# Kernel optimization log

Measured on AMD Instinct MI355X. Metric: run time of the kernel, lower is better.

Reference implementation:

```python
import jax, jax.numpy as jnp
import numpy as np

B, S, T = 64, 64, 20
E, H, V, K = 512, 1024, 32000, 100
L, W = 50, 8
NEG = -1e9


def lstm_cell(x, h, c, Wih, Whh, bih, bhh):
    # PyTorch gate order: input, forget, cell, output
    g = x @ Wih.T + h @ Whh.T + bih + bhh
    i, f, gg, o = jnp.split(g, 4, axis=-1)
    c = jax.nn.sigmoid(f) * c + jax.nn.sigmoid(i) * jnp.tanh(gg)
    h = jax.nn.sigmoid(o) * jnp.tanh(c)
    return h, c


def setup_inputs():
    key = jax.random.key(0)
    ks = jax.random.split(key, 32)
    rn = lambda k, shp, s=0.02: (s * jax.random.normal(k, shp)).astype(jnp.float32)
    embed_W = jax.random.normal(ks[0], (V, E), dtype=jnp.float32).at[0].set(0.0)  # padding_idx 0
    return {
        'src_seqs': jax.random.randint(ks[1], (B, S), 1, V),
        'src_lengths': jax.random.randint(ks[2], (B,), S // 2, S + 1),
        'trg_seqs': jax.random.randint(ks[3], (B, T), 1, V),
        'ctc_seqs': jax.random.randint(ks[4], (B, L, W), 1, V),
        'ctc_lengths': jax.random.randint(ks[5], (B,), 1, L + 1),
        'embed_W': embed_W,
        'enc_Wih': rn(ks[6], (4 * H, E)), 'enc_Whh': rn(ks[7], (4 * H, H)),
        'enc_bih': rn(ks[8], (4 * H,)), 'enc_bhh': rn(ks[9], (4 * H,)),
        'dec_Wih': rn(ks[10], (4 * H, E + H)), 'dec_Whh': rn(ks[11], (4 * H, H)),
        'dec_bih': rn(ks[12], (4 * H,)), 'dec_bhh': rn(ks[13], (4 * H,)),
        'qk_W': rn(ks[14], (K, E)), 'qk_b': rn(ks[15], (K,)),
        'qv_W': rn(ks[16], (H, E)), 'qv_b': rn(ks[17], (H,)),
        'ak_W': rn(ks[18], (K, H)), 'ak_b': rn(ks[19], (K,)),
        'out_W': rn(ks[20], (E, 2 * H)), 'out_b': rn(ks[21], (E,)),
        'wd_b': rn(ks[22], (V,)),
        'hf1_W': rn(ks[23], (2 * H, H)), 'hf1_b': rn(ks[24], (2 * H,)),
        'hf2_W': rn(ks[25], (H, 2 * H)), 'hf2_b': rn(ks[26], (H,)),
        'cf1_W': rn(ks[27], (2 * H, H)), 'cf1_b': rn(ks[28], (2 * H,)),
        'cf2_W': rn(ks[29], (H, 2 * H)), 'cf2_b': rn(ks[30], (H,)),
    }


def forward(floats, ints):
    (embed_W, enc_Wih, enc_Whh, enc_bih, enc_bhh, dec_Wih, dec_Whh, dec_bih, dec_bhh,
     qk_W, qk_b, qv_W, qv_b, ak_W, ak_b, out_W, out_b, wd_b,
     hf1_W, hf1_b, hf2_W, hf2_b, cf1_W, cf1_b, cf2_W, cf2_b) = floats
    src_seqs, src_lengths, trg_seqs, ctc_seqs, ctc_lengths = ints

    src_embed = embed_W[src_seqs]  # [B,S,E]

    # ---- encoder LSTM (seq-first scan); packed-seq final state = state at src_lengths-1 ----
    def enc_step(carry, x_t):
        h, c = lstm_cell(x_t, carry[0], carry[1], enc_Wih, enc_Whh, enc_bih, enc_bhh)
        return (h, c), (h, c)
    z = jnp.zeros((B, H), jnp.float32)
    _, (hs, cs) = jax.lax.scan(enc_step, (z, z), src_embed.transpose(1, 0, 2))  # [S,B,H]
    idx = src_lengths - 1
    h_last = hs[idx, jnp.arange(B)]
    c_last = cs[idx, jnp.arange(B)]

    # ---- init_hidden: MLP transforms of encoder final state ----
    h0 = jax.nn.relu(h_last @ hf1_W.T + hf1_b) @ hf2_W.T + hf2_b
    c0 = jax.nn.relu(c_last @ cf1_W.T + cf1_b) @ cf2_W.T + cf2_b

    # ---- persona context: mean word embedding per context item ----
    ctx_embed = embed_W[ctc_seqs].mean(axis=2)       # [B,L,E]
    q_key = jnp.tanh(ctx_embed @ qk_W.T + qk_b)      # [B,L,K]
    q_value = ctx_embed @ qv_W.T + qv_b              # [B,L,H]
    mask = jnp.arange(L)[None, :] < ctc_lengths[:, None]  # [B,L]

    ans_embed = embed_W[trg_seqs]                    # [B,T,E]

    # ---- decoder: per-step attention + LSTM + tied-vocab projection ----
    def dec_step(carry, x_t):
        h, c = carry
        a_key = jnp.tanh(h @ ak_W.T + ak_b)                      # [B,K]
        e = jnp.einsum('blk,bk->bl', q_key, a_key)
        w = jax.nn.softmax(jnp.where(mask, e, NEG), axis=1)
        ctx = jnp.einsum('bl,blh->bh', w, q_value)               # [B,H]
        h, c = lstm_cell(jnp.concatenate([x_t, ctx], -1), h, c,
                         dec_Wih, dec_Whh, dec_bih, dec_bhh)
        ox = jnp.concatenate([h, ctx], -1) @ out_W.T + out_b     # [B,E]
        logits = ox @ embed_W.T + wd_b                           # tied weights, [B,V]
        return (h, c), logits

    # teacher forcing (sampling_rate=1.0, T-1 <= max_len-2)
    _, logits = jax.lax.scan(dec_step, (h0, c0), ans_embed[:, :T - 1].transpose(1, 0, 2))
    return logits.transpose(1, 0, 2)  # [B, T-1, V]


def reference(src_seqs, src_lengths, trg_seqs, ctc_seqs, ctc_lengths, embed_W, enc_Wih, enc_Whh, enc_bih, enc_bhh, dec_Wih, dec_Whh, dec_bih, dec_bhh, qk_W, qk_b, qv_W, qv_b, ak_W, ak_b, out_W, out_b, wd_b, hf1_W, hf1_b, hf2_W, hf2_b, cf1_W, cf1_b, cf2_W, cf2_b):
    floats = (embed_W, enc_Wih, enc_Whh, enc_bih, enc_bhh, dec_Wih, dec_Whh, dec_bih, dec_bhh,
              qk_W, qk_b, qv_W, qv_b, ak_W, ak_b, out_W, out_b, wd_b,
              hf1_W, hf1_b, hf2_W, hf2_b, cf1_W, cf1_b, cf2_W, cf2_b)
    ints = (src_seqs, src_lengths, trg_seqs, ctc_seqs, ctc_lengths)
    return forward(floats, ints)
```

## Files before the change

### kernel.cpp

```cpp
#include <hip/hip_runtime.h>
#include <hip/hip_bf16.h>
#include <math.h>

#define Bn 64
#define Sn 64
#define Tn 20
#define TD 19
#define En 512
#define Hn 1024
#define Vn 32000
#define Kan 100
#define Lnn 50
#define Wnn 8

typedef __attribute__((ext_vector_type(8))) short short8v;
typedef __attribute__((ext_vector_type(4))) float floatx4;
typedef __hip_bfloat16 bf16;
typedef unsigned long long ull;

__device__ __forceinline__ float sigm(float x) { return 1.0f / (1.0f + expf(-x)); }
__device__ __forceinline__ float bfb2f(unsigned int u) {
    return __builtin_bit_cast(float, u << 16);
}
__device__ __forceinline__ unsigned short f2bfb(float f) {
    return __builtin_bit_cast(unsigned short, __float2bfloat16(f));
}

#define ALOAD(p)     __hip_atomic_load((p), __ATOMIC_RELAXED, __HIP_MEMORY_SCOPE_AGENT)
#define ASTORE(p, v) __hip_atomic_store((p), (v), __ATOMIC_RELAXED, __HIP_MEMORY_SCOPE_AGENT)

__device__ __forceinline__ uint4 gload16(const void* p) {
    uint4 v;
    asm volatile("global_load_dwordx4 %0, %1, off sc0 sc1"
                 : "=v"(v) : "v"(p));
    return v;
}
#define GWAIT() asm volatile("s_waitcnt vmcnt(0)" ::: "memory")

__device__ __forceinline__ void gbar(unsigned int* c, int tid) {
    __builtin_amdgcn_sched_barrier(0);
    __syncthreads();
    if (tid == 0) {
        __hip_atomic_fetch_add(c, 1u, __ATOMIC_RELAXED, __HIP_MEMORY_SCOPE_AGENT);
        while (__hip_atomic_load(c, __ATOMIC_RELAXED, __HIP_MEMORY_SCOPE_AGENT) < 128u) {
            __builtin_amdgcn_s_sleep(1);
        }
    }
    __syncthreads();
    __builtin_amdgcn_sched_barrier(0);
}

#define EOFF(r, p) (((r) << 5) + ((((p) ^ ((r) & 3))) << 3))

__device__ __forceinline__ int aswz(int row, int p) {
    return row * 32 + (((p ^ ((row >> 1) & 3))) << 3);
}
__device__ __forceinline__ int wswz(int col, int s, int K) {
    return col * K + (((s & ~7) | ((s & 7) ^ (col & 7))) << 3);
}

template<int GATHER, int EPI, int ACT>
__global__ __launch_bounds__(256)
void mgemm(const bf16* __restrict__ A, int lda, const int* __restrict__ tok,
           const bf16* __restrict__ W, int ldw,
           const float* __restrict__ b1, const float* __restrict__ b2,
           float* __restrict__ C, int ldc,
           bf16* __restrict__ Cbf, int ldcbf,
           int M, int N, int K)
{
    __shared__ bf16 As[128 * 32];
    __shared__ bf16 Bs[128 * 32];
    const int tid = threadIdx.x;
    const int lane = tid & 63, wv = tid >> 6;
    const int wm = wv >> 1, wn = wv & 1;
    const int n0 = (EPI == 2 ? blockIdx.y : blockIdx.x) * 128;
    const int r0 = (EPI == 2 ? blockIdx.x : blockIdx.y) * 128;
    const int srow = tid >> 2, sp = tid & 3;

    const int ra_r0 = r0 + srow, ra_r1 = r0 + srow + 64;
    const bool av0 = ra_r0 < M, av1 = ra_r1 < M;
    const size_t arow0 = (size_t)(av0 ? (GATHER ? tok[ra_r0] : ra_r0) : 0) * lda;
    const size_t arow1 = (size_t)(av1 ? (GATHER ? tok[ra_r1] : ra_r1) : 0) * lda;
    const size_t wrow0 = (size_t)(n0 + srow) * ldw;
    const size_t wrow1 = (size_t)(n0 + srow + 64) * ldw;

    const uint4 z4 = make_uint4(0, 0, 0, 0);
    uint4 ra0, ra1, rb0, rb1;
#define LOADTILE_G(k0) do { \
        ra0 = av0 ? *((const uint4*)(A + arow0 + (k0)) + sp) : z4; \
        ra1 = av1 ? *((const uint4*)(A + arow1 + (k0)) + sp) : z4; \
        rb0 = *((const uint4*)(W + wrow0 + (k0)) + sp); \
        rb1 = *((const uint4*)(W + wrow1 + (k0)) + sp); \
    } while (0)

    floatx4 acc[4][4] = {};
    const int lr = lane & 15, p2 = lane >> 4;

    LOADTILE_G(0);
    for (int k0 = 0; k0 < K; k0 += 32) {
        __syncthreads();
        *(uint4*)(As + EOFF(srow, sp)) = ra0;
        *(uint4*)(As + EOFF(srow + 64, sp)) = ra1;
        *(uint4*)(Bs + EOFF(srow, sp)) = rb0;
        *(uint4*)(Bs + EOFF(srow + 64, sp)) = rb1;
        __syncthreads();
        if (k0 + 32 < K) LOADTILE_G(k0 + 32);
        short8v aF[4], bF[4];
#pragma unroll
        for (int mf = 0; mf < 4; ++mf)
            aF[mf] = *(const short8v*)(As + EOFF(wm * 64 + mf * 16 + lr, p2));
#pragma unroll
        for (int nf = 0; nf < 4; ++nf)
            bF[nf] = *(const short8v*)(Bs + EOFF(wn * 64 + nf * 16 + lr, p2));
#pragma unroll
        for (int mf = 0; mf < 4; ++mf)
#pragma unroll
            for (int nf = 0; nf < 4; ++nf)
                acc[mf][nf] = __builtin_amdgcn_mfma_f32_16x16x32_bf16(
                    aF[mf], bF[nf], acc[mf][nf], 0, 0, 0);
    }
#undef LOADTILE_G

    const int rbase = r0 + wm * 64 + (lane >> 4) * 4;
    const int nbase = n0 + wn * 64 + (lane & 15);
#pragma unroll
    for (int nf = 0; nf < 4; ++nf) {
        const int n = nbase + nf * 16;
        if (n >= N) continue;
        float bias = b1 ? b1[n] : 0.0f;
        if (b2) bias += b2[n];
#pragma unroll
        for (int mf = 0; mf < 4; ++mf) {
#pragma unroll
            for (int i = 0; i < 4; ++i) {
                const int r = rbase + mf * 16 + i;
                if (r >= M) continue;
                float v = acc[mf][nf][i] + bias;
                if (ACT == 1) v = tanhf(v);
                if (ACT == 2) v = fmaxf(v, 0.0f);
                if (EPI == 2) {
                    int b = r & 63, t = r >> 6;
                    C[(size_t)(b * TD + t) * Vn + n] = v;
                } else {
                    if (C) C[(size_t)r * ldc + n] = v;
                    if (Cbf) Cbf[(size_t)r * ldcbf + n] = __float2bfloat16(v);
                }
            }
        }
    }
}

struct EncP {
    const bf16* Wp;
    const bf16* Xg;
    bf16* hA; bf16* hB;
    const int* len;
    bf16* hlast; bf16* clast;
    unsigned int* cnt;
};

__global__ __launch_bounds__(512, 1)
void enc_persist(EncP p)
{
    __shared__ bf16 Ws_l[32 * 1024];
    __shared__ bf16 Asb[2][64 * 32];
    __shared__ float Gs[64][33];
    const int tid = threadIdx.x;
    const int lane = tid & 63, wv = tid >> 6;
    const int mf = wv >> 1, nf = wv & 1;
    const int blk = blockIdx.x;
    const int n0 = blk * 32;

    for (int idx = tid; idx < 32 * 128; idx += 512) {
        int col = idx >> 7, s = idx & 127;
        uint4 v = *(const uint4*)(p.Wp + (size_t)(n0 + col) * 1024 + s * 8);
        *(uint4*)(Ws_l + wswz(col, s, 1024)) = v;
    }

    const int b = tid >> 3, jl = tid & 7;
    const int j = (n0 >> 2) + jl;
    float c_reg = 0.0f;
    const int hw = b * 256 + blk * 2 + (jl >> 2);
    if ((lane & 3) == 0) ASTORE((ull*)p.hA + hw, 0ull);
    const int mylen = p.len[b];

    const int arow = mf * 16 + (lane & 15);
    const int a_rd = aswz(arow, lane >> 4);
    const int bcol = nf * 16 + (lane & 15);
    const int bbase = bcol * 1024;
    const int srow = tid >> 2, sp = tid & 3;
    const int a_wr = aswz(srow, sp);
    const int gr = mf * 16 + (lane >> 4) * 4;
    const int gc = nf * 16 + (lane & 15);

    gbar(p.cnt + 0, tid);

    for (int t = 0; t < Sn; ++t) {
        const bf16* hsrc = (t & 1) ? p.hB : p.hA;
        bf16* hn = (t & 1) ? p.hA : p.hB;
        const bf16* xg = p.Xg + ((size_t)t * Bn + b) * 4096;
        float xf0 = __bfloat162float(xg[j]);
        float xf1 = __bfloat162float(xg[1024 + j]);
        float xf2 = __bfloat162float(xg[2048 + j]);
        float xf3 = __bfloat162float(xg[3072 + j]);
        floatx4 acc = {};
        uint4 ra;
        if (tid < 256) ra = gload16(hsrc + srow * 1024 + sp * 8);
        __syncthreads();
        if (tid < 256) { GWAIT(); *(uint4*)(Asb[0] + a_wr) = ra; }
        if (tid < 256) ra = gload16(hsrc + srow * 1024 + 32 + sp * 8);
        for (int k0 = 0; k0 < 1024; k0 += 32) {
            const int cur = (k0 >> 5) & 1;
            __syncthreads();
            if (k0 + 32 < 1024) {
                if (tid < 256) { GWAIT(); *(uint4*)(Asb[cur ^ 1] + a_wr) = ra; }
                if (k0 + 64 < 1024 && tid < 256)
                    ra = gload16(hsrc + srow * 1024 + k0 + 64 + sp * 8);
            }
            short8v af = *(const short8v*)(Asb[cur] + a_rd);
            int s = (k0 >> 3) + (lane >> 4);
            short8v bfr = *(const short8v*)(Ws_l + bbase +
                             (((s & ~7) | ((s & 7) ^ (bcol & 7))) << 3));
            acc = __builtin_amdgcn_mfma_f32_16x16x32_bf16(af, bfr, acc, 0, 0, 0);
        }
        Gs[gr + 0][gc] = acc[0];
        Gs[gr + 1][gc] = acc[1];
        Gs[gr + 2][gc] = acc[2];
        Gs[gr + 3][gc] = acc[3];
        __syncthreads();
        float gi = Gs[b][jl * 4 + 0] + xf0;
        float gf = Gs[b][jl * 4 + 1] + xf1;
        float gg = Gs[b][jl * 4 + 2] + xf2;
        float go = Gs[b][jl * 4 + 3] + xf3;
        float cnv = sigm(gf) * c_reg + sigm(gi) * tanhf(gg);
        float hnv = sigm(go) * tanhf(cnv);
        c_reg = cnv;
        if (t == mylen - 1) {
            p.hlast[b * 1024 + j] = __float2bfloat16(hnv);
            p.clast[b * 1024 + j] = __float2bfloat16(cnv);
        }
        {
            unsigned int q0 = f2bfb(hnv);
            unsigned int q1 = __shfl_down(q0, 1);
            unsigned int q2 = __shfl_down(q0, 2);
            unsigned int q3 = __shfl_down(q0, 3);
            if ((lane & 3) == 0)
                ASTORE((ull*)hn + hw,
                       (ull)q0 | ((ull)q1 << 16) | ((ull)q2 << 32) | ((ull)q3 << 48));
        }
        if (t < Sn - 1) gbar(p.cnt + 1 + t, tid);
    }
}

struct DecP {
    const bf16* Wp;
    const bf16* Xg;
    bf16* hA; bf16* hB;
    bf16* ctx;
    const float* c0;
    const float* akW; const float* akb;
    const float* qkey;
    const float* qval;
    const int* clen;
    bf16* hcat;
    unsigned int* cnt;
};

__global__ __launch_bounds__(512, 1)
void dec_persist(DecP p)
{
    __shared__ bf16 Ws_l[32 * 2048];
    __shared__ bf16 Asb[2][64 * 32];
    __shared__ float Gs[64][33];
    __shared__ float akey[104];
    __shared__ float ebuf[52];
    __shared__ float wts[52];
    float* hsh = &Gs[0][0];

    const int tid = threadIdx.x;
    const int lane = tid & 63, wv = tid >> 6;
    const int mf = wv >> 1, nf = wv & 1;
    const int blk = blockIdx.x;
    const int n0 = blk * 32;

    for (int idx = tid; idx < 32 * 256; idx += 512) {
        int col = idx >> 8, s = idx & 255;
        uint4 v = *(const uint4*)(p.Wp + (size_t)(n0 + col) * 2048 + s * 8);
        *(uint4*)(Ws_l + wswz(col, s, 2048)) = v;
    }

    const int b = tid >> 3, jl = tid & 7;
    const int j = (n0 >> 2) + jl;
    float c_reg = p.c0[b * 1024 + j];
    const int hw = b * 256 + blk * 2 + (jl >> 2);

    const int arow = mf * 16 + (lane & 15);
    const int a_rd = aswz(arow, lane >> 4);
    const int bcol = nf * 16 + (lane & 15);
    const int bbase = bcol * 2048;
    const int srow = tid >> 2, sp = tid & 3;
    const int a_wr = aswz(srow, sp);
    const int gr = mf * 16 + (lane >> 4) * 4;
    const int gc = nf * 16 + (lane & 15);

    gbar(p.cnt + 65, tid);

    for (int t = 0; t < TD; ++t) {
        const bf16* hsrc = (t & 1) ? p.hB : p.hA;
        bf16* hn = (t & 1) ? p.hA : p.hB;
        const bf16* ctxsrc = p.ctx;
        const ull* hq = (const ull*)hsrc;

        if (blockIdx.x < 64) {
            const int ab = blockIdx.x;
            if (tid < 256) {
                ull v = ALOAD(hq + ab * 256 + tid);
                hsh[tid * 4 + 0] = bfb2f((unsigned)(v & 0xffff));
                hsh[tid * 4 + 1] = bfb2f((unsigned)((v >> 16) & 0xffff));
                hsh[tid * 4 + 2] = bfb2f((unsigned)((v >> 32) & 0xffff));
                hsh[tid * 4 + 3] = bfb2f((unsigned)(v >> 48));
            }
            __syncthreads();
            for (int k = wv; k < Kan; k += 8) {
                float s = 0.0f;
#pragma unroll
                for (int m = 0; m < 16; ++m)
                    s += hsh[lane + m * 64] * p.akW[(size_t)k * 1024 + lane + m * 64];
                for (int off = 32; off; off >>= 1) s += __shfl_down(s, off);
                if (lane == 0) akey[k] = tanhf(s + p.akb[k]);
            }
            __syncthreads();
            for (int l = wv; l < Lnn; l += 8) {
                const float* qr = p.qkey + (size_t)(ab * Lnn + l) * Kan;
                float s = qr[lane] * akey[lane];
                if (lane < Kan - 64) s += qr[lane + 64] * akey[lane + 64];
                for (int off = 32; off; off >>= 1) s += __shfl_down(s, off);
                if (lane == 0) ebuf[l] = s;
            }
            __syncthreads();
            if (wv == 0) {
                int len = p.clen[ab];
                float e = (lane < Lnn) ? (lane < len ? ebuf[lane] : -1e9f)
                                       : -3.402823466e38f;
                float mx = e;
                for (int off = 32; off; off >>= 1) mx = fmaxf(mx, __shfl_xor(mx, off));
                float pr = (lane < Lnn) ? expf(e - mx) : 0.0f;
                float sm = pr;
                for (int off = 32; off; off >>= 1) sm += __shfl_xor(sm, off);
                if (lane < Lnn) wts[lane] = pr / sm;
            }
            __syncthreads();
#pragma unroll
            for (int pass = 0; pass < 2; ++pass) {
                int jj = tid + pass * 512;
                float s = 0.0f;
                for (int l = 0; l < Lnn; ++l)
                    s += wts[l] * p.qval[((size_t)ab * Lnn + l) * 1024 + jj];
                unsigned short cb = f2bfb(s);
                p.hcat[((size_t)t * Bn + ab) * 2048 + 1024 + jj] =
                    __builtin_bit_cast(bf16, cb);
                unsigned int q0 = cb;
                unsigned int q1 = __shfl_down(q0, 1);
                unsigned int q2 = __shfl_down(q0, 2);
                unsigned int q3 = __shfl_down(q0, 3);
                if ((lane & 3) == 0)
                    ASTORE((ull*)p.ctx + ab * 256 + pass * 128 + (tid >> 2),
                           (ull)q0 | ((ull)q1 << 16) | ((ull)q2 << 32) | ((ull)q3 << 48));
            }
        }
        gbar(p.cnt + 66 + 2 * t, tid);

        const bf16* xg = p.Xg + ((size_t)t * Bn + b) * 4096;
        float xf0 = __bfloat162float(xg[j]);
        float xf1 = __bfloat162float(xg[1024 + j]);
        float xf2 = __bfloat162float(xg[2048 + j]);
        float xf3 = __bfloat162float(xg[3072 + j]);
        floatx4 acc = {};
        uint4 ra;
        if (tid < 256) ra = gload16(hsrc + srow * 1024 + sp * 8);
        __syncthreads();
        if (tid < 256) { GWAIT(); *(uint4*)(Asb[0] + a_wr) = ra; }
        if (tid < 256) ra = gload16(hsrc + srow * 1024 + 32 + sp * 8);
        for (int k0 = 0; k0 < 2048; k0 += 32) {
            const int cur = (k0 >> 5) & 1;
            __syncthreads();
            if (k0 + 32 < 2048) {
                if (tid < 256) { GWAIT(); *(uint4*)(Asb[cur ^ 1] + a_wr) = ra; }
                if (k0 + 64 < 2048 && tid < 256) {
                    const int kn = k0 + 64;
                    const bf16* asrc = (kn < 1024) ? hsrc : ctxsrc;
                    ra = gload16(asrc + srow * 1024 + (kn & 1023) + sp * 8);
                }
            }
            short8v af = *(const short8v*)(Asb[cur] + a_rd);
            int s = (k0 >> 3) + (lane >> 4);
            short8v bfr = *(const short8v*)(Ws_l + bbase +
                             (((s & ~7) | ((s & 7) ^ (bcol & 7))) << 3));
            acc = __builtin_amdgcn_mfma_f32_16x16x32_bf16(af, bfr, acc, 0, 0, 0);
        }
        Gs[gr + 0][gc] = acc[0];
        Gs[gr + 1][gc] = acc[1];
        Gs[gr + 2][gc] = acc[2];
        Gs[gr + 3][gc] = acc[3];
        __syncthreads();
        float gi = Gs[b][jl * 4 + 0] + xf0;
        float gf = Gs[b][jl * 4 + 1] + xf1;
        float gg = Gs[b][jl * 4 + 2] + xf2;
        float go = Gs[b][jl * 4 + 3] + xf3;
        float cnv = sigm(gf) * c_reg + sigm(gi) * tanhf(gg);
        float hnv = sigm(go) * tanhf(cnv);
        c_reg = cnv;
        bf16 hb = __float2bfloat16(hnv);
        p.hcat[((size_t)t * Bn + b) * 2048 + j] = hb;
        {
            unsigned int q0 = f2bfb(hnv);
            unsigned int q1 = __shfl_down(q0, 1);
            unsigned int q2 = __shfl_down(q0, 2);
            unsigned int q3 = __shfl_down(q0, 3);
            if ((lane & 3) == 0)
                ASTORE((ull*)hn + hw,
                       (ull)q0 | ((ull)q1 << 16) | ((ull)q2 << 32) | ((ull)q3 << 48));
        }
        if (t < TD - 1) gbar(p.cnt + 66 + 2 * t + 1, tid);
    }
}

__global__ __launch_bounds__(128)
void ctx_embed_kernel(const int* __restrict__ ctc, const float* __restrict__ embed,
                      bf16* __restrict__ ctxe_bf)
{
    const int row = blockIdx.x;
    const int tid = threadIdx.x;
    __shared__ int toks[8];
    if (tid < 8) toks[tid] = ctc[row * Wnn + tid];
    __syncthreads();
#pragma unroll
    for (int p = 0; p < 4; ++p) {
        int e = tid + p * 128;
        float s = 0.0f;
#pragma unroll
        for (int w = 0; w < 8; ++w) s += embed[(size_t)toks[w] * En + e];
        ctxe_bf[(size_t)row * En + e] = __float2bfloat16(s * 0.125f);
    }
}

__global__ void prep_tokens(const int* __restrict__ src, const int* __restrict__ trg,
                            int* __restrict__ tokA, int* __restrict__ tokD)
{
    int i = blockIdx.x * 256 + threadIdx.x;
    if (i < Bn * Sn) tokA[i] = src[(i & 63) * Sn + (i >> 6)];
    if (i < TD * Bn) tokD[i] = trg[(i & 63) * Tn + (i >> 6)];
}

__global__ void conv_f2b(const float* __restrict__ src, bf16* __restrict__ dst, int n)
{
    int i = (blockIdx.x * 256 + threadIdx.x) * 4;
    if (i >= n) return;
    float4 v = *(const float4*)(src + i);
    dst[i + 0] = __float2bfloat16(v.x);
    dst[i + 1] = __float2bfloat16(v.y);
    dst[i + 2] = __float2bfloat16(v.z);
    dst[i + 3] = __float2bfloat16(v.w);
}

__global__ void pad_qkw(const float* __restrict__ qkW, bf16* __restrict__ Wp)
{
    int i = blockIdx.x * 256 + threadIdx.x;
    int r = i >> 9;
    Wp[i] = __float2bfloat16(r < Kan ? qkW[(size_t)r * En + (i & 511)] : 0.0f);
}

__global__ void perm_enc(const float* __restrict__ Whh, bf16* __restrict__ Wp)
{
    int row = blockIdx.x;
    int j = row >> 2, g = row & 3;
    const float* s = Whh + (size_t)(g * 1024 + j) * 1024;
    bf16* d = Wp + (size_t)row * 1024;
    for (int e = threadIdx.x; e < 1024; e += 256) d[e] = __float2bfloat16(s[e]);
}

__global__ void perm_dec(const float* __restrict__ Whh, const float* __restrict__ Wih,
                         bf16* __restrict__ Wp)
{
    int row = blockIdx.x;
    int j = row >> 2, g = row & 3;
    int sr = g * 1024 + j;
    const float* s1 = Whh + (size_t)sr * 1024;
    const float* s2 = Wih + (size_t)sr * 1536 + 512;
    bf16* d = Wp + (size_t)row * 2048;
    for (int e = threadIdx.x; e < 1024; e += 256) {
        d[e] = __float2bfloat16(s1[e]);
        d[1024 + e] = __float2bfloat16(s2[e]);
    }
}

extern "C" void kernel_launch(void* const* d_in, const int* in_sizes, int n_in,
                              void* d_out, int out_size, void* d_ws, size_t ws_size,
                              hipStream_t stream)
{
    (void)in_sizes; (void)n_in; (void)out_size; (void)ws_size;
    const int*   src     = (const int*)d_in[0];
    const int*   srclen  = (const int*)d_in[1];
    const int*   trg     = (const int*)d_in[2];
    const int*   ctc     = (const int*)d_in[3];
    const int*   ctclen  = (const int*)d_in[4];
    const float* embed   = (const float*)d_in[5];
    const float* enc_Wih = (const float*)d_in[6];
    const float* enc_Whh = (const float*)d_in[7];
    const float* enc_bih = (const float*)d_in[8];
    const float* enc_bhh = (const float*)d_in[9];
    const float* dec_Wih = (const float*)d_in[10];
    const float* dec_Whh = (const float*)d_in[11];
    const float* dec_bih = (const float*)d_in[12];
    const float* dec_bhh = (const float*)d_in[13];
    const float* qkW     = (const float*)d_in[14];
    const float* qkb     = (const float*)d_in[15];
    const float* qvW     = (const float*)d_in[16];
    const float* qvb     = (const float*)d_in[17];
    const float* akW     = (const float*)d_in[18];
    const float* akb     = (const float*)d_in[19];
    const float* outW    = (const float*)d_in[20];
    const float* outb    = (const float*)d_in[21];
    const float* wdb     = (const float*)d_in[22];
    const float* hf1W    = (const float*)d_in[23];
    const float* hf1b    = (const float*)d_in[24];
    const float* hf2W    = (const float*)d_in[25];
    const float* hf2b    = (const float*)d_in[26];
    const float* cf1W    = (const float*)d_in[27];
    const float* cf1b    = (const float*)d_in[28];
    const float* cf2W    = (const float*)d_in[29];
    const float* cf2b    = (const float*)d_in[30];
    float* out = (float*)d_out;

    char* ws = (char*)d_ws;
    size_t off = 0;
    auto alloc = [&](size_t bytes) -> void* {
        void* p = ws + off;
        off += (bytes + 255) & ~(size_t)255;
        return p;
    };
    bf16*  embed_bf  = (bf16*)alloc((size_t)Vn * En * 2);
    bf16*  encWih_bf = (bf16*)alloc((size_t)4096 * En * 2);
    bf16*  decWih_bf = (bf16*)alloc((size_t)4096 * 1536 * 2);
    bf16*  qvW_bf    = (bf16*)alloc((size_t)Hn * En * 2);
    bf16*  outW_bf   = (bf16*)alloc((size_t)En * 2048 * 2);
    bf16*  Wenc_p    = (bf16*)alloc((size_t)4096 * 1024 * 2);
    bf16*  Wdec_p    = (bf16*)alloc((size_t)4096 * 2048 * 2);
    bf16*  hf1W_bf   = (bf16*)alloc((size_t)2048 * 1024 * 2);
    bf16*  hf2W_bf   = (bf16*)alloc((size_t)1024 * 2048 * 2);
    bf16*  cf1W_bf   = (bf16*)alloc((size_t)2048 * 1024 * 2);
    bf16*  cf2W_bf   = (bf16*)alloc((size_t)1024 * 2048 * 2);
    bf16*  qkWp      = (bf16*)alloc((size_t)128 * En * 2);
    bf16*  Xenc_bf   = (bf16*)alloc((size_t)Sn * Bn * 4096 * 2);
    bf16*  Xdec_bf   = (bf16*)alloc((size_t)TD * Bn * 4096 * 2);
    float* qkey      = (float*)alloc((size_t)Bn * Lnn * Kan * 4);
    float* qval      = (float*)alloc((size_t)Bn * Lnn * Hn * 4);
    bf16*  ctxe_bf   = (bf16*)alloc((size_t)Bn * Lnn * En * 2);
    bf16*  henc0     = (bf16*)alloc((size_t)Bn * Hn * 2);
    bf16*  henc1     = (bf16*)alloc((size_t)Bn * Hn * 2);
    bf16*  hdec0     = (bf16*)alloc((size_t)Bn * Hn * 2);
    bf16*  hdec1     = (bf16*)alloc((size_t)Bn * Hn * 2);
    bf16*  ctxbuf    = (bf16*)alloc((size_t)Bn * Hn * 2);
    float* cbuf0     = (float*)alloc((size_t)Bn * Hn * 4);
    bf16*  hlast_bf  = (bf16*)alloc((size_t)Bn * Hn * 2);
    bf16*  clast_bf  = (bf16*)alloc((size_t)Bn * Hn * 2);
    bf16*  t2h_bf    = (bf16*)alloc((size_t)Bn * 2048 * 2);
    bf16*  t2c_bf    = (bf16*)alloc((size_t)Bn * 2048 * 2);
    int*   tokA      = (int*)alloc((size_t)Bn * Sn * 4);
    int*   tokD      = (int*)alloc((size_t)TD * Bn * 4);
    unsigned int* cnt = (unsigned int*)alloc(128 * 4);
    bf16*  hcat_bf   = Xenc_bf;
    bf16*  ox_bf     = Xenc_bf + (size_t)TD * Bn * 2048;

    hipMemsetAsync(cnt, 0, 128 * 4, stream);

    conv_f2b<<<(Vn * En) / 1024, 256, 0, stream>>>(embed, embed_bf, Vn * En);
    conv_f2b<<<(4096 * En) / 1024, 256, 0, stream>>>(enc_Wih, encWih_bf, 4096 * En);
    conv_f2b<<<(4096 * 1536) / 1024, 256, 0, stream>>>(dec_Wih, decWih_bf, 4096 * 1536);
    conv_f2b<<<(Hn * En) / 1024, 256, 0, stream>>>(qvW, qvW_bf, Hn * En);
    conv_f2b<<<(En * 2048) / 1024, 256, 0, stream>>>(outW, outW_bf, En * 2048);
    conv_f2b<<<(2048 * 1024) / 1024, 256, 0, stream>>>(hf1W, hf1W_bf, 2048 * 1024);
    conv_f2b<<<(1024 * 2048) / 1024, 256, 0, stream>>>(hf2W, hf2W_bf, 1024 * 2048);
    conv_f2b<<<(2048 * 1024) / 1024, 256, 0, stream>>>(cf1W, cf1W_bf, 2048 * 1024);
    conv_f2b<<<(1024 * 2048) / 1024, 256, 0, stream>>>(cf2W, cf2W_bf, 1024 * 2048);
    pad_qkw<<<(128 * En) / 256, 256, 0, stream>>>(qkW, qkWp);
    perm_enc<<<4096, 256, 0, stream>>>(enc_Whh, Wenc_p);
    perm_dec<<<4096, 256, 0, stream>>>(dec_Whh, dec_Wih, Wdec_p);
    prep_tokens<<<16, 256, 0, stream>>>(src, trg, tokA, tokD);
    ctx_embed_kernel<<<Bn * Lnn, 128, 0, stream>>>(ctc, embed, ctxe_bf);

    mgemm<1, 0, 0><<<dim3(32, 32), 256, 0, stream>>>(
        embed_bf, En, tokA, encWih_bf, En, enc_bih, enc_bhh,
        nullptr, 0, Xenc_bf, 4096, Bn * Sn, 4096, En);
    mgemm<1, 0, 0><<<dim3(32, 10), 256, 0, stream>>>(
        embed_bf, En, tokD, decWih_bf, 1536, dec_bih, dec_bhh,
        nullptr, 0, Xdec_bf, 4096, TD * Bn, 4096, En);
    mgemm<0, 0, 0><<<dim3(8, 25), 256, 0, stream>>>(
        ctxe_bf, En, nullptr, qvW_bf, En, qvb, nullptr,
        qval, Hn, nullptr, 0, Bn * Lnn, Hn, En);
    mgemm<0, 0, 1><<<dim3(1, 25), 256, 0, stream>>>(
        ctxe_bf, En, nullptr, qkWp, En, qkb, nullptr,
        qkey, Kan, nullptr, 0, Bn * Lnn, Kan, En);

    {
        EncP ep;
        ep.Wp = Wenc_p; ep.Xg = Xenc_bf; ep.hA = henc0; ep.hB = henc1;
        ep.len = srclen; ep.hlast = hlast_bf; ep.clast = clast_bf; ep.cnt = cnt;
        void* args[] = {&ep};
        hipLaunchCooperativeKernel((void*)enc_persist, dim3(128), dim3(512),
                                   args, 0, stream);
    }

    mgemm<0, 0, 2><<<dim3(16, 1), 256, 0, stream>>>(
        hlast_bf, Hn, nullptr, hf1W_bf, Hn, hf1b, nullptr,
        nullptr, 0, t2h_bf, 2048, Bn, 2048, Hn);
    mgemm<0, 0, 0><<<dim3(8, 1), 256, 0, stream>>>(
        t2h_bf, 2048, nullptr, hf2W_bf, 2048, hf2b, nullptr,
        nullptr, 0, hdec0, 1024, Bn, Hn, 2048);
    mgemm<0, 0, 2><<<dim3(16, 1), 256, 0, stream>>>(
        clast_bf, Hn, nullptr, cf1W_bf, Hn, cf1b, nullptr,
        nullptr, 0, t2c_bf, 2048, Bn, 2048, Hn);
    mgemm<0, 0, 0><<<dim3(8, 1), 256, 0, stream>>>(
        t2c_bf, 2048, nullptr, cf2W_bf, 2048, cf2b, nullptr,
        cbuf0, Hn, nullptr, 0, Bn, Hn, 2048);

    {
        DecP dp;
        dp.Wp = Wdec_p; dp.Xg = Xdec_bf; dp.hA = hdec0; dp.hB = hdec1;
        dp.ctx = ctxbuf; dp.c0 = cbuf0;
        dp.akW = akW; dp.akb = akb; dp.qkey = qkey; dp.qval = qval;
        dp.clen = ctclen; dp.hcat = hcat_bf; dp.cnt = cnt;
        void* args[] = {&dp};
        hipLaunchCooperativeKernel((void*)dec_persist, dim3(128), dim3(512),
                                   args, 0, stream);
    }

    mgemm<0, 0, 0><<<dim3(4, 10), 256, 0, stream>>>(
        hcat_bf, 2048, nullptr, outW_bf, 2048, outb, nullptr,
        nullptr, 0, ox_bf, En, TD * Bn, En, 2048);
    mgemm<0, 2, 0><<<dim3(10, Vn / 128), 256, 0, stream>>>(
        ox_bf, En, nullptr, embed_bf, En, wdb, nullptr,
        out, 0, nullptr, 0, TD * Bn, Vn, En);
}
```

Measured before the change: 2.816 ms.

## Deepen recurrent h-load prefetch to 4-stage register ring, add ILP to attention dots

The encoder and decoder recurrent GEMV loops now keep four outstanding global loads of the hidden state in a register ring and wait with vmcnt(3) instead of vmcnt(0). This lets more memory latency overlap with the MFMA steps, and the loops are fully unrolled. The attention-key dot product computes two keys per wavefront iteration, and the context weighted sum uses two accumulators, both to add instruction-level parallelism. The cost is higher register pressure and larger code from the unrolling.

After: 3.278 ms. 1.16x slower.

```diff
diff --git a/kernel.cpp b/kernel.cpp
--- a/kernel.cpp
+++ b/kernel.cpp
@@ -35,7 +35,8 @@
                  : "=v"(v) : "v"(p));
     return v;
 }
-#define GWAIT() asm volatile("s_waitcnt vmcnt(0)" ::: "memory")
+#define WAITC3() asm volatile("s_waitcnt vmcnt(3)" ::: "memory")
+#define WAITC0() asm volatile("s_waitcnt vmcnt(0)" ::: "memory")
 
 __device__ __forceinline__ void gbar(unsigned int* c, int tid) {
     __builtin_amdgcn_sched_barrier(0);
@@ -192,33 +193,39 @@
     const int a_wr = aswz(srow, sp);
     const int gr = mf * 16 + (lane >> 4) * 4;
     const int gc = nf * 16 + (lane & 15);
+    const int p2 = lane >> 4;
 
     gbar(p.cnt + 0, tid);
 
+    const int NT = 32;
     for (int t = 0; t < Sn; ++t) {
         const bf16* hsrc = (t & 1) ? p.hB : p.hA;
         bf16* hn = (t & 1) ? p.hA : p.hB;
+        const bf16* hrow = hsrc + srow * 1024 + sp * 8;
         const bf16* xg = p.Xg + ((size_t)t * Bn + b) * 4096;
         float xf0 = __bfloat162float(xg[j]);
         float xf1 = __bfloat162float(xg[1024 + j]);
         float xf2 = __bfloat162float(xg[2048 + j]);
         float xf3 = __bfloat162float(xg[3072 + j]);
         floatx4 acc = {};
-        uint4 ra;
-        if (tid < 256) ra = gload16(hsrc + srow * 1024 + sp * 8);
-        __syncthreads();
-        if (tid < 256) { GWAIT(); *(uint4*)(Asb[0] + a_wr) = ra; }
-        if (tid < 256) ra = gload16(hsrc + srow * 1024 + 32 + sp * 8);
-        for (int k0 = 0; k0 < 1024; k0 += 32) {
-            const int cur = (k0 >> 5) & 1;
+        uint4 ring[4];
+        if (tid < 256) {
+#pragma unroll
+            for (int q = 0; q < 4; ++q) ring[q] = gload16(hrow + q * 32);
+            WAITC3();
+            *(uint4*)(Asb[0] + a_wr) = ring[0];
+            ring[0] = gload16(hrow + 4 * 32);
+        }
+#pragma unroll
+        for (int i = 0; i < NT; ++i) {
             __syncthreads();
-            if (k0 + 32 < 1024) {
-                if (tid < 256) { GWAIT(); *(uint4*)(Asb[cur ^ 1] + a_wr) = ra; }
-                if (k0 + 64 < 1024 && tid < 256)
-                    ra = gload16(hsrc + srow * 1024 + k0 + 64 + sp * 8);
-            }
-            short8v af = *(const short8v*)(Asb[cur] + a_rd);
-            int s = (k0 >> 3) + (lane >> 4);
+            if (i + 1 < NT && tid < 256) {
+                if (i + 1 <= NT - 4) { WAITC3(); } else { WAITC0(); }
+                *(uint4*)(Asb[(i + 1) & 1] + a_wr) = ring[(i + 1) & 3];
+                if (i + 5 < NT) ring[(i + 1) & 3] = gload16(hrow + (i + 5) * 32);
+            }
+            short8v af = *(const short8v*)(Asb[i & 1] + a_rd);
+            int s = 4 * i + p2;
             short8v bfr = *(const short8v*)(Ws_l + bbase +
                              (((s & ~7) | ((s & 7) ^ (bcol & 7))) << 3));
             acc = __builtin_amdgcn_mfma_f32_16x16x32_bf16(af, bfr, acc, 0, 0, 0);
@@ -302,9 +309,11 @@
     const int a_wr = aswz(srow, sp);
     const int gr = mf * 16 + (lane >> 4) * 4;
     const int gc = nf * 16 + (lane & 15);
+    const int p2 = lane >> 4;
 
     gbar(p.cnt + 65, tid);
 
+    const int NT = 64;
     for (int t = 0; t < TD; ++t) {
         const bf16* hsrc = (t & 1) ? p.hB : p.hA;
         bf16* hn = (t & 1) ? p.hA : p.hB;
@@ -321,13 +330,25 @@
                 hsh[tid * 4 + 3] = bfb2f((unsigned)(v >> 48));
             }
             __syncthreads();
-            for (int k = wv; k < Kan; k += 8) {
-                float s = 0.0f;
-#pragma unroll
-                for (int m = 0; m < 16; ++m)
-                    s += hsh[lane + m * 64] * p.akW[(size_t)k * 1024 + lane + m * 64];
-                for (int off = 32; off; off >>= 1) s += __shfl_down(s, off);
-                if (lane == 0) akey[k] = tanhf(s + p.akb[k]);
+            for (int k = wv; k < Kan; k += 16) {
+                const bool two = (k + 8) < Kan;
+                const float* w0 = p.akW + (size_t)k * 1024;
+                const float* w1 = p.akW + (size_t)(two ? k + 8 : k) * 1024;
+                float s0 = 0.0f, s1 = 0.0f;
+#pragma unroll
+                for (int m = 0; m < 16; ++m) {
+                    float hv = hsh[lane + m * 64];
+                    s0 += hv * w0[lane + m * 64];
+                    s1 += hv * w1[lane + m * 64];
+                }
+                for (int off = 32; off; off >>= 1) {
+                    s0 += __shfl_down(s0, off);
+                    s1 += __shfl_down(s1, off);
+                }
+                if (lane == 0) {
+                    akey[k] = tanhf(s0 + p.akb[k]);
+                    if (two) akey[k + 8] = tanhf(s1 + p.akb[k + 8]);
+                }
             }
             __syncthreads();
             for (int l = wv; l < Lnn; l += 8) {
@@ -353,10 +374,14 @@
 #pragma unroll
             for (int pass = 0; pass < 2; ++pass) {
                 int jj = tid + pass * 512;
-                float s = 0.0f;
-                for (int l = 0; l < Lnn; ++l)
-                    s += wts[l] * p.qval[((size_t)ab * Lnn + l) * 1024 + jj];
-                unsigned short cb = f2bfb(s);
+                const float* qv = p.qval + (size_t)ab * Lnn * 1024 + jj;
+                float s0 = 0.0f, s1 = 0.0f;
+#pragma unroll
+                for (int l = 0; l < Lnn; l += 2) {
+                    s0 += wts[l] * qv[(size_t)l * 1024];
+                    s1 += wts[l + 1] * qv[(size_t)(l + 1) * 1024];
+                }
+                unsigned short cb = f2bfb(s0 + s1);
                 p.hcat[((size_t)t * Bn + ab) * 2048 + 1024 + jj] =
                     __builtin_bit_cast(bf16, cb);
                 unsigned int q0 = cb;
@@ -375,25 +400,30 @@
         float xf1 = __bfloat162float(xg[1024 + j]);
         float xf2 = __bfloat162float(xg[2048 + j]);
         float xf3 = __bfloat162float(xg[3072 + j]);
+        const bf16* hrow = hsrc + srow * 1024 + sp * 8;
+        const bf16* crow = ctxsrc + srow * 1024 + sp * 8;
         floatx4 acc = {};
-        uint4 ra;
-        if (tid < 256) ra = gload16(hsrc + srow * 1024 + sp * 8);
-        __syncthreads();
-        if (tid < 256) { GWAIT(); *(uint4*)(Asb[0] + a_wr) = ra; }
-        if (tid < 256) ra = gload16(hsrc + srow * 1024 + 32 + sp * 8);
-        for (int k0 = 0; k0 < 2048; k0 += 32) {
-            const int cur = (k0 >> 5) & 1;
+        uint4 ring[4];
+        if (tid < 256) {
+#pragma unroll
+            for (int q = 0; q < 4; ++q) ring[q] = gload16(hrow + q * 32);
+            WAITC3();
+            *(uint4*)(Asb[0] + a_wr) = ring[0];
+            ring[0] = gload16(hrow + 4 * 32);
+        }
+#pragma unroll
+        for (int i = 0; i < NT; ++i) {
             __syncthreads();
-            if (k0 + 32 < 2048) {
-                if (tid < 256) { GWAIT(); *(uint4*)(Asb[cur ^ 1] + a_wr) = ra; }
-                if (k0 + 64 < 2048 && tid < 256) {
-                    const int kn = k0 + 64;
-                    const bf16* asrc = (kn < 1024) ? hsrc : ctxsrc;
-                    ra = gload16(asrc + srow * 1024 + (kn & 1023) + sp * 8);
+            if (i + 1 < NT && tid < 256) {
+                if (i + 1 <= NT - 4) { WAITC3(); } else { WAITC0(); }
+                *(uint4*)(Asb[(i + 1) & 1] + a_wr) = ring[(i + 1) & 3];
+                if (i + 5 < NT) {
+                    const bf16* src = (i + 5 < 32) ? hrow : crow;
+                    ring[(i + 1) & 3] = gload16(src + ((i + 5) & 31) * 32);
                 }
             }
-            short8v af = *(const short8v*)(Asb[cur] + a_rd);
-            int s = (k0 >> 3) + (lane >> 4);
+            short8v af = *(const short8v*)(Asb[i & 1] + a_rd);
+            int s = 4 * i + p2;
             short8v bfr = *(const short8v*)(Ws_l + bbase +
                              (((s & ~7) | ((s & 7) ^ (bcol & 7))) << 3));
             acc = __builtin_amdgcn_mfma_f32_16x16x32_bf16(af, bfr, acc, 0, 0, 0);
```

## Replace decoder per-step context grid barrier with counter wait overlapping h-part GEMM

Applied to the files above, without the earlier changes.

In the decoder's persistent loop, the grid-wide barrier after the attention/context computation is replaced by a per-step arrival counter that the 64 attention blocks increment. All blocks start the recurrent GEMM over the hidden-state half immediately and wait on the counter only before loading the context half. This overlaps the attention phase with half of the gate GEMM and removes one full grid barrier per step. The A-tile loads now use relaxed atomic 64-bit loads instead of the sc0/sc1 inline asm loads, and the context reduction over L is split into two accumulators. Counter indices are renumbered, which risks collisions with other counters if the layout is wrong.

Measured after the change: 2.809 ms. Within noise of the previous version (-0.3%).

```diff
diff --git a/kernel.cpp b/kernel.cpp
--- a/kernel.cpp
+++ b/kernel.cpp
@@ -28,6 +28,15 @@
 
 #define ALOAD(p)     __hip_atomic_load((p), __ATOMIC_RELAXED, __HIP_MEMORY_SCOPE_AGENT)
 #define ASTORE(p, v) __hip_atomic_store((p), (v), __ATOMIC_RELAXED, __HIP_MEMORY_SCOPE_AGENT)
+
+__device__ __forceinline__ uint4 aload16(const ull* base, int ullIdx) {
+    ull u0 = ALOAD(base + ullIdx);
+    ull u1 = ALOAD(base + ullIdx + 1);
+    uint4 v;
+    v.x = (unsigned)u0; v.y = (unsigned)(u0 >> 32);
+    v.z = (unsigned)u1; v.w = (unsigned)(u1 >> 32);
+    return v;
+}
 
 __device__ __forceinline__ uint4 gload16(const void* p) {
     uint4 v;
@@ -198,6 +207,7 @@
     for (int t = 0; t < Sn; ++t) {
         const bf16* hsrc = (t & 1) ? p.hB : p.hA;
         bf16* hn = (t & 1) ? p.hA : p.hB;
+        const bf16* hrow = hsrc + srow * 1024 + sp * 8;
         const bf16* xg = p.Xg + ((size_t)t * Bn + b) * 4096;
         float xf0 = __bfloat162float(xg[j]);
         float xf1 = __bfloat162float(xg[1024 + j]);
@@ -205,17 +215,17 @@
         float xf3 = __bfloat162float(xg[3072 + j]);
         floatx4 acc = {};
         uint4 ra;
-        if (tid < 256) ra = gload16(hsrc + srow * 1024 + sp * 8);
+        if (tid < 256) ra = gload16(hrow);
         __syncthreads();
         if (tid < 256) { GWAIT(); *(uint4*)(Asb[0] + a_wr) = ra; }
-        if (tid < 256) ra = gload16(hsrc + srow * 1024 + 32 + sp * 8);
+        if (tid < 256) ra = gload16(hrow + 32);
         for (int k0 = 0; k0 < 1024; k0 += 32) {
             const int cur = (k0 >> 5) & 1;
             __syncthreads();
             if (k0 + 32 < 1024) {
                 if (tid < 256) { GWAIT(); *(uint4*)(Asb[cur ^ 1] + a_wr) = ra; }
                 if (k0 + 64 < 1024 && tid < 256)
-                    ra = gload16(hsrc + srow * 1024 + k0 + 64 + sp * 8);
+                    ra = gload16(hrow + k0 + 64);
             }
             short8v af = *(const short8v*)(Asb[cur] + a_rd);
             int s = (k0 >> 3) + (lane >> 4);
@@ -302,17 +312,19 @@
     const int a_wr = aswz(srow, sp);
     const int gr = mf * 16 + (lane >> 4) * 4;
     const int gc = nf * 16 + (lane & 15);
-
-    gbar(p.cnt + 65, tid);
+    const int sbase = srow * 256 + sp * 2;
+
+    gbar(p.cnt + 64, tid);
 
     for (int t = 0; t < TD; ++t) {
         const bf16* hsrc = (t & 1) ? p.hB : p.hA;
         bf16* hn = (t & 1) ? p.hA : p.hB;
-        const bf16* ctxsrc = p.ctx;
         const ull* hq = (const ull*)hsrc;
-
-        if (blockIdx.x < 64) {
-            const int ab = blockIdx.x;
+        const ull* cq = (const ull*)p.ctx;
+        unsigned int* ctxc = p.cnt + 90 + t;
+
+        if (blk < 64) {
+            const int ab = blk;
             if (tid < 256) {
                 ull v = ALOAD(hq + ab * 256 + tid);
                 hsh[tid * 4 + 0] = bfb2f((unsigned)(v & 0xffff));
@@ -353,10 +365,13 @@
 #pragma unroll
             for (int pass = 0; pass < 2; ++pass) {
                 int jj = tid + pass * 512;
-                float s = 0.0f;
-                for (int l = 0; l < Lnn; ++l)
-                    s += wts[l] * p.qval[((size_t)ab * Lnn + l) * 1024 + jj];
-                unsigned short cb = f2bfb(s);
+                const float* qv = p.qval + (size_t)ab * Lnn * 1024 + jj;
+                float s0 = 0.0f, s1 = 0.0f;
+                for (int l = 0; l < Lnn; l += 2) {
+                    s0 += wts[l] * qv[(size_t)l * 1024];
+                    s1 += wts[l + 1] * qv[(size_t)(l + 1) * 1024];
+                }
+                unsigned short cb = f2bfb(s0 + s1);
                 p.hcat[((size_t)t * Bn + ab) * 2048 + 1024 + jj] =
                     __builtin_bit_cast(bf16, cb);
                 unsigned int q0 = cb;
@@ -367,8 +382,11 @@
                     ASTORE((ull*)p.ctx + ab * 256 + pass * 128 + (tid >> 2),
                            (ull)q0 | ((ull)q1 << 16) | ((ull)q2 << 32) | ((ull)q3 << 48));
             }
-        }
-        gbar(p.cnt + 66 + 2 * t, tid);
+            __syncthreads();
+            if (tid == 0)
+                __hip_atomic_fetch_add(ctxc, 1u, __ATOMIC_RELAXED,
+                                       __HIP_MEMORY_SCOPE_AGENT);
+        }
 
         const bf16* xg = p.Xg + ((size_t)t * Bn + b) * 4096;
         float xf0 = __bfloat162float(xg[j]);
@@ -377,23 +395,32 @@
         float xf3 = __bfloat162float(xg[3072 + j]);
         floatx4 acc = {};
         uint4 ra;
-        if (tid < 256) ra = gload16(hsrc + srow * 1024 + sp * 8);
+        if (tid < 256) ra = aload16(hq, sbase);
         __syncthreads();
-        if (tid < 256) { GWAIT(); *(uint4*)(Asb[0] + a_wr) = ra; }
-        if (tid < 256) ra = gload16(hsrc + srow * 1024 + 32 + sp * 8);
-        for (int k0 = 0; k0 < 2048; k0 += 32) {
-            const int cur = (k0 >> 5) & 1;
+        if (tid < 256) *(uint4*)(Asb[0] + a_wr) = ra;
+        if (tid < 256) ra = aload16(hq, sbase + 8);
+        for (int i = 0; i < 64; ++i) {
+            if (i == 30) {
+                __builtin_amdgcn_sched_barrier(0);
+                if (tid == 0) {
+                    while (__hip_atomic_load(ctxc, __ATOMIC_RELAXED,
+                                             __HIP_MEMORY_SCOPE_AGENT) < 64u) {
+                        __builtin_amdgcn_s_sleep(1);
+                    }
+                }
+                __syncthreads();
+                __builtin_amdgcn_sched_barrier(0);
+            }
             __syncthreads();
-            if (k0 + 32 < 2048) {
-                if (tid < 256) { GWAIT(); *(uint4*)(Asb[cur ^ 1] + a_wr) = ra; }
-                if (k0 + 64 < 2048 && tid < 256) {
-                    const int kn = k0 + 64;
-                    const bf16* asrc = (kn < 1024) ? hsrc : ctxsrc;
-                    ra = gload16(asrc + srow * 1024 + (kn & 1023) + sp * 8);
+            if (i + 1 < 64 && tid < 256) {
+                *(uint4*)(Asb[(i + 1) & 1] + a_wr) = ra;
+                if (i + 2 < 64) {
+                    const ull* aq = (i + 2 < 32) ? hq : cq;
+                    ra = aload16(aq, sbase + (((i + 2) & 31) << 3));
                 }
             }
-            short8v af = *(const short8v*)(Asb[cur] + a_rd);
-            int s = (k0 >> 3) + (lane >> 4);
+            short8v af = *(const short8v*)(Asb[i & 1] + a_rd);
+            int s = 4 * i + (lane >> 4);
             short8v bfr = *(const short8v*)(Ws_l + bbase +
                              (((s & ~7) | ((s & 7) ^ (bcol & 7))) << 3));
             acc = __builtin_amdgcn_mfma_f32_16x16x32_bf16(af, bfr, acc, 0, 0, 0);
@@ -421,7 +448,7 @@
                 ASTORE((ull*)hn + hw,
                        (ull)q0 | ((ull)q1 << 16) | ((ull)q2 << 32) | ((ull)q3 << 48));
         }
-        if (t < TD - 1) gbar(p.cnt + 66 + 2 * t + 1, tid);
+        if (t < TD - 1) gbar(p.cnt + 65 + t, tid);
     }
 }
 
```
